# Optimization experiments

Measured on AMD Instinct MI355X. Metric: run time of the kernel, lower is better.

Reference implementation:

```python
import jax, jax.numpy as jnp
import numpy as np

EPS = 1e-5


def conv3x3(x, w, b):
    # x [B,C,H,W], w [O,C,3,3], stride 1, pad 1
    y = jax.lax.conv_general_dilated(x, w, (1, 1), ((1, 1), (1, 1)),
                                     dimension_numbers=('NCHW', 'OIHW', 'NCHW'))
    return y + b[None, :, None, None]


def bilinear_gather(x, py, px):
    # x [B,C,H,W]; sampling locations py,px [B,K,H,W] -> [B,C,K,H,W]
    # Zero padding outside the image (matches deform_conv CUDA semantics:
    # out-of-bound corner values contribute 0).
    B, C, H, W = x.shape
    K = py.shape[1]
    x_flat = x.reshape(B, C, H * W)
    y0 = jnp.floor(py)
    x0 = jnp.floor(px)
    out = jnp.zeros((B, C, K, H, W), x.dtype)
    for dy in (0.0, 1.0):
        for dx in (0.0, 1.0):
            yi = y0 + dy
            xi = x0 + dx
            wgt = (1.0 - jnp.abs(py - yi)) * (1.0 - jnp.abs(px - xi))  # [B,K,H,W]
            valid = (yi >= 0) & (yi <= H - 1) & (xi >= 0) & (xi <= W - 1)
            idx = (jnp.clip(yi, 0, H - 1).astype(jnp.int32) * W
                   + jnp.clip(xi, 0, W - 1).astype(jnp.int32)).reshape(B, -1)
            vals = jax.vmap(lambda xf, i: xf[:, i])(x_flat, idx)  # [B,C,K*H*W]
            out = out + (wgt * valid)[:, None] * vals.reshape(B, C, K, H, W)
    return out


def setup_inputs() -> dict:
    key = jax.random.key(0)
    k1, k2, k3 = jax.random.split(key, 3)
    B, C, O, H, W = 4, 64, 64, 128, 128
    x = jax.random.normal(k1, (B, C, H, W), jnp.float32)
    # offset predictor: small init so predicted offsets are modest (realistic)
    off_w = 0.01 * jax.random.normal(k2, (18, C, 3, 3), jnp.float32)
    off_b = jnp.zeros((18,), jnp.float32)
    dc_w = jax.random.normal(k3, (O, C, 3, 3), jnp.float32) / np.sqrt(C * 9)
    dc_b = jnp.zeros((O,), jnp.float32)
    gamma = jnp.ones((O,), jnp.float32)
    beta = jnp.zeros((O,), jnp.float32)
    return {"x": x, "off_w": off_w, "off_b": off_b, "dc_w": dc_w,
            "dc_b": dc_b, "gamma": gamma, "beta": beta}


def reference(x, off_w, off_b, dc_w, dc_b, gamma, beta):
    B, C, H, W = x.shape
    O = dc_w.shape[0]
    K = 9  # 3x3 kernel
    offset = conv3x3(x, off_w, off_b)              # [B,18,H,W]
    off = offset.reshape(B, K, 2, H, W)            # (dy,dx) per kernel tap, row-major
    dyo, dxo = off[:, :, 0], off[:, :, 1]          # [B,K,H,W]
    k = (jnp.arange(3) - 1).astype(x.dtype)        # kernel taps {-1,0,1}
    kgy = jnp.repeat(k, 3)                         # [9] row-major y offsets
    kgx = jnp.tile(k, 3)                           # [9] row-major x offsets
    hh = jnp.arange(H, dtype=x.dtype)
    ww = jnp.arange(W, dtype=x.dtype)
    # stride 1, pad 1: base point = out_pos - 1 + tap; pad is folded into kgy/kgx
    py = hh[None, None, :, None] + kgy[None, :, None, None] + dyo
    px = ww[None, None, None, :] + kgx[None, :, None, None] + dxo
    sampled = bilinear_gather(x, py, px)           # [B,C,K,H,W]
    y = jnp.einsum('ock,bckhw->bohw', dc_w.reshape(O, C, K), sampled)
    y = y + dc_b[None, :, None, None]
    # BatchNorm2d (training mode: biased batch statistics)
    mu = y.mean(axis=(0, 2, 3), keepdims=True)
    var = y.var(axis=(0, 2, 3), keepdims=True)
    yn = (y - mu) * jax.lax.rsqrt(var + EPS)
    return jax.nn.relu(yn * gamma[None, :, None, None] + beta[None, :, None, None])
```

## Files before the change

kernel.cpp:

```cpp
#include <hip/hip_runtime.h>

#define HH 128
#define WW 128
#define HWSZ (HH * WW)
#define CC 64
#define OO 64
#define BB 4
#define NOFF 18
#define KK 576

#define WS_BG     0
#define WS_BGO    18432
#define WS_SUMS   27648
#define WS_SUMSQ  27712
#define WS_YBUF   27776

typedef __attribute__((ext_vector_type(8))) short short8;
typedef __attribute__((ext_vector_type(4))) int int4v;
typedef __attribute__((ext_vector_type(4))) float f32x4;

__device__ inline unsigned bf16rne(float f) {
  unsigned u = __float_as_uint(f);
  u += 0x7fff + ((u >> 16) & 1);
  return u >> 16;
}

__global__ __launch_bounds__(256) void prep_kernel(
    const float* __restrict__ x, const float* __restrict__ off_w,
    const float* __restrict__ dc_w, unsigned int* __restrict__ xTu,
    int* __restrict__ Bg, int* __restrict__ Bgo, float* __restrict__ sums) {
  int bid = blockIdx.x;
  if (bid < BB * HH) {
    __shared__ float T[CC][WW + 1];
    int b = bid >> 7, h = bid & 127;
    int tw = threadIdx.x & 127, th = threadIdx.x >> 7;
    const float* xp = x + (size_t)b * CC * HWSZ + h * WW;
#pragma unroll 8
    for (int i = 0; i < 32; ++i) {
      int c = i * 2 + th;
      T[c][tw] = xp[c * HWSZ + tw];
    }
    __syncthreads();
    int c2 = threadIdx.x & 31, wq = threadIdx.x >> 5;
    unsigned int* op = xTu + ((size_t)(b * HH + h) * WW) * 32;
#pragma unroll 8
    for (int i = 0; i < 16; ++i) {
      int w = i * 8 + wq;
      unsigned pk = bf16rne(T[2 * c2][w]) | (bf16rne(T[2 * c2 + 1][w]) << 16);
      op[w * 32 + c2] = pk;
    }
  } else {
    int pb = bid - BB * HH;
    int tid = pb * 256 + threadIdx.x;
    int stride = 64 * 256;
    for (int i = tid; i < 72 * 64 * 4; i += stride) {
      int j = i & 3, o = (i >> 2) & 63, g = i >> 8;
      int k2 = g * 4 + j, t = k2 >> 5, jj = k2 & 31;
      unsigned lo = bf16rne(dc_w[o * KK + (2 * jj) * 9 + t]);
      unsigned hi = bf16rne(dc_w[o * KK + (2 * jj + 1) * 9 + t]);
      Bg[i] = (int)(lo | (hi << 16));
    }
    for (int i = tid; i < 72 * 32 * 4; i += stride) {
      int j = i & 3, o = (i >> 2) & 31, g = i >> 7;
      int k2 = g * 4 + j, t = k2 >> 5, jj = k2 & 31;
      unsigned pk = 0;
      if (o < NOFF) {
        unsigned lo = bf16rne(off_w[o * KK + (2 * jj) * 9 + t]);
        unsigned hi = bf16rne(off_w[o * KK + (2 * jj + 1) * 9 + t]);
        pk = lo | (hi << 16);
      }
      Bgo[i] = (int)pk;
    }
    if (tid < 128) sums[tid] = 0.0f;
  }
}

__global__ __launch_bounds__(256) void fused_kernel(
    const unsigned int* __restrict__ xTu, const int* __restrict__ Bg,
    const int* __restrict__ Bgo, const float* __restrict__ off_b,
    const float* __restrict__ dc_b, float* __restrict__ ybuf,
    float* __restrict__ sums, float* __restrict__ sumsq) {
  __shared__ __align__(16) int A[4 * 16 * 100];
  __shared__ __align__(16) int M[4 * 144 * 4];
  __shared__ float offL[4][NOFF][16];

  int cg = threadIdx.x >> 6, lane = threadIdx.x & 63;
  int b = blockIdx.x >> 8, rem = blockIdx.x & 255;
  int h = rem >> 1, w0 = (rem & 1) * 64;
  int hw0 = h * WW + w0;
  int p0 = cg * 16;
  int n16 = lane & 15, q = lane >> 4;
  int pg = lane >> 3, part = lane & 7;
  const unsigned int* xbu = xTu + (size_t)b * HWSZ * 32;

  f32x4 acc2[2] = {f32x4{0, 0, 0, 0}, f32x4{0, 0, 0, 0}};
#pragma unroll 1
  for (int chunk = 0; chunk < 3; ++chunk) {
    int cy = h + chunk - 1;
    bool vy = (cy >= 0) && (cy < HH);
    int cys = min(max(cy, 0), HH - 1);
#pragma unroll
    for (int tl = 0; tl < 3; ++tl) {
#pragma unroll
      for (int i = 0; i < 2; ++i) {
        int px = i * 8 + pg;
        int cx = w0 + p0 + px + tl - 1;
        bool v = vy && (cx >= 0) && (cx < WW);
        int cxs = min(max(cx, 0), WW - 1);
        int4v val = *(const int4v*)&xbu[(cys * WW + cxs) * 32 + part * 4];
        if (!v) { val.x = 0; val.y = 0; val.z = 0; val.w = 0; }
        *(int4v*)&A[(p0 + px) * 100 + tl * 32 + part * 4] = val;
      }
    }
#pragma unroll 1
    for (int kk = 0; kk < 6; ++kk) {
      int4v av = *(const int4v*)&A[(p0 + n16) * 100 + kk * 16 + q * 4];
      short8 af = __builtin_bit_cast(short8, av);
      int g = chunk * 24 + kk * 4 + q;
#pragma unroll
      for (int nt = 0; nt < 2; ++nt) {
        int4v bv = *(const int4v*)&Bgo[(g * 32 + nt * 16 + n16) * 4];
        short8 bfr = __builtin_bit_cast(short8, bv);
        acc2[nt] = __builtin_amdgcn_mfma_f32_16x16x32_bf16(af, bfr, acc2[nt], 0, 0, 0);
      }
    }
  }
#pragma unroll
  for (int nt = 0; nt < 2; ++nt) {
    int o = nt * 16 + n16;
    if (o < NOFF) {
      float bv = off_b[o];
#pragma unroll
      for (int r = 0; r < 4; ++r) offL[cg][o][q * 4 + r] = acc2[nt][r] + bv;
    }
  }

  int* Mw = M + cg * 144 * 4;
#pragma unroll
  for (int it = 0; it < 3; ++it) {
    int m = it * 64 + lane;
    if (m < 144) {
      int pxl = (unsigned)m / 9u;
      int t = m - pxl * 9;
      float dy = offL[cg][2 * t][pxl];
      float dx = offL[cg][2 * t + 1][pxl];
      float py = (float)(h + t / 3 - 1) + dy;
      float pxf = (float)(w0 + p0 + pxl + (t % 3) - 1) + dx;
      float fy0 = floorf(py), fx0 = floorf(pxf);
      float ay = py - fy0, ax = pxf - fx0;
      int iy0 = (int)fy0, ix0 = (int)fx0;
      int iy1 = iy0 + 1, ix1 = ix0 + 1;
      float wy0 = 1.0f - ay, wy1 = ay, wx0 = 1.0f - ax, wx1 = ax;
      if (!(iy0 >= 0 && iy0 < HH)) wy0 = 0.0f;
      if (!(iy1 >= 0 && iy1 < HH)) wy1 = 0.0f;
      if (!(ix0 >= 0 && ix0 < WW)) wx0 = 0.0f;
      if (!(ix1 >= 0 && ix1 < WW)) wx1 = 0.0f;
      int cy0 = min(max(iy0, 0), HH - 1), cy1 = min(max(iy1, 0), HH - 1);
      int cx0 = min(max(ix0, 0), WW - 1), cx1 = min(max(ix1, 0), WW - 1);
      int4v mv;
      mv.x = (cy0 * WW + cx0) | ((cy0 * WW + cx1) << 16);
      mv.y = (cy1 * WW + cx0) | ((cy1 * WW + cx1) << 16);
      mv.z = (int)(bf16rne(wy0 * wx0) | (bf16rne(wy0 * wx1) << 16));
      mv.w = (int)(bf16rne(wy1 * wx0) | (bf16rne(wy1 * wx1) << 16));
      *(int4v*)&Mw[m * 4] = mv;
    }
  }

  int p = lane >> 5;
  int c2 = lane & 31;
  f32x4 acc[4] = {f32x4{0,0,0,0}, f32x4{0,0,0,0}, f32x4{0,0,0,0}, f32x4{0,0,0,0}};
#pragma unroll 1
  for (int chunk = 0; chunk < 3; ++chunk) {
#pragma unroll 1
    for (int tl = 0; tl < 3; ++tl) {
#pragma unroll 4
      for (int pp = 0; pp < 16; pp += 2) {
        int pxl = pp + p;
        int4v mv = *(const int4v*)&Mw[(pxl * 9 + chunk * 3 + tl) * 4];
        unsigned o00 = mv.x & 0xffff, o01 = ((unsigned)mv.x) >> 16;
        unsigned o10 = mv.y & 0xffff, o11 = ((unsigned)mv.y) >> 16;
        unsigned d00 = xbu[o00 * 32 + c2];
        unsigned d01 = xbu[o01 * 32 + c2];
        unsigned d10 = xbu[o10 * 32 + c2];
        unsigned d11 = xbu[o11 * 32 + c2];
        float w00 = __uint_as_float(((unsigned)mv.z) << 16);
        float w01 = __uint_as_float(((unsigned)mv.z) & 0xffff0000u);
        float w10 = __uint_as_float(((unsigned)mv.w) << 16);
        float w11 = __uint_as_float(((unsigned)mv.w) & 0xffff0000u);
        float slo = w00 * __uint_as_float(d00 << 16);
        slo = fmaf(w01, __uint_as_float(d01 << 16), slo);
        slo = fmaf(w10, __uint_as_float(d10 << 16), slo);
        slo = fmaf(w11, __uint_as_float(d11 << 16), slo);
        float shi = w00 * __uint_as_float(d00 & 0xffff0000u);
        shi = fmaf(w01, __uint_as_float(d01 & 0xffff0000u), shi);
        shi = fmaf(w10, __uint_as_float(d10 & 0xffff0000u), shi);
        shi = fmaf(w11, __uint_as_float(d11 & 0xffff0000u), shi);
        unsigned pk = __builtin_amdgcn_perm(
            __float_as_uint(shi) + 0x8000u,
            __float_as_uint(slo) + 0x8000u, 0x07060302u);
        A[(p0 + pxl) * 100 + tl * 32 + c2] = (int)pk;
      }
    }
#pragma unroll 1
    for (int kk = 0; kk < 6; ++kk) {
      int4v av = *(const int4v*)&A[(p0 + n16) * 100 + kk * 16 + q * 4];
      short8 af = __builtin_bit_cast(short8, av);
      int g = chunk * 24 + kk * 4 + q;
#pragma unroll
      for (int nt = 0; nt < 4; ++nt) {
        int4v bv = *(const int4v*)&Bg[(g * 64 + nt * 16 + n16) * 4];
        short8 bfr = __builtin_bit_cast(short8, bv);
        acc[nt] = __builtin_amdgcn_mfma_f32_16x16x32_bf16(af, bfr, acc[nt], 0, 0, 0);
      }
    }
  }

  float* SW = (float*)&A[cg * 1600];
#pragma unroll
  for (int nt = 0; nt < 4; ++nt) {
    int o = nt * 16 + n16;
    float bv = dc_b[o];
    f32x4 r;
    float s = 0.0f, ss = 0.0f;
#pragma unroll
    for (int r0 = 0; r0 < 4; ++r0) {
      r[r0] = acc[nt][r0] + bv;
      s += r[r0];
      ss += r[r0] * r[r0];
    }
    *(f32x4*)(ybuf + (size_t)(b * OO + o) * HWSZ + hw0 + p0 + q * 4) = r;
    s += __shfl_xor(s, 16);  s += __shfl_xor(s, 32);
    ss += __shfl_xor(ss, 16); ss += __shfl_xor(ss, 32);
    if (lane < 16) {
      SW[nt * 16 + lane] = s;
      SW[64 + nt * 16 + lane] = ss;
    }
  }
  __syncthreads();
  if (threadIdx.x < 64) {
    float ts = 0.0f, tq = 0.0f;
#pragma unroll
    for (int wv = 0; wv < 4; ++wv) {
      const float* Sv = (const float*)&A[wv * 1600];
      ts += Sv[threadIdx.x];
      tq += Sv[64 + threadIdx.x];
    }
    atomicAdd(&sums[threadIdx.x], ts);
    atomicAdd(&sumsq[threadIdx.x], tq);
  }
}

__global__ __launch_bounds__(256) void norm_kernel(
    const float* __restrict__ ybuf, const float* __restrict__ sums,
    const float* __restrict__ sumsq, const float* __restrict__ gamma,
    const float* __restrict__ beta, float* __restrict__ out) {
  int gid = blockIdx.x * 256 + threadIdx.x;
  int flat = gid << 2;
  int o = (flat >> 14) & 63;
  const float invN = 1.0f / (float)(BB * HWSZ);
  float mean = sums[o] * invN;
  float var = sumsq[o] * invN - mean * mean;
  float rstd = rsqrtf(var + 1e-5f);
  float g = gamma[o] * rstd;
  float bta = beta[o] - mean * g;
  float4 v = ((const float4*)ybuf)[gid];
  float4 r;
  r.x = fmaxf(v.x * g + bta, 0.0f);
  r.y = fmaxf(v.y * g + bta, 0.0f);
  r.z = fmaxf(v.z * g + bta, 0.0f);
  r.w = fmaxf(v.w * g + bta, 0.0f);
  ((float4*)out)[gid] = r;
}

extern "C" void kernel_launch(void* const* d_in, const int* in_sizes, int n_in,
                              void* d_out, int out_size, void* d_ws, size_t ws_size,
                              hipStream_t stream) {
  const float* x     = (const float*)d_in[0];
  const float* off_w = (const float*)d_in[1];
  const float* off_b = (const float*)d_in[2];
  const float* dc_w  = (const float*)d_in[3];
  const float* dc_b  = (const float*)d_in[4];
  const float* gamma = (const float*)d_in[5];
  const float* beta  = (const float*)d_in[6];
  float* ws = (float*)d_ws;
  int*   Bg     = (int*)(ws + WS_BG);
  int*   Bgo    = (int*)(ws + WS_BGO);
  float* sums   = ws + WS_SUMS;
  float* sumsq  = ws + WS_SUMSQ;
  float* ybuf   = ws + WS_YBUF;
  float* out = (float*)d_out;
  unsigned int* xTu = (unsigned int*)d_out;

  prep_kernel<<<BB * HH + 64, 256, 0, stream>>>(x, off_w, dc_w, xTu, Bg, Bgo, sums);
  fused_kernel<<<BB * HWSZ / 64, 256, 0, stream>>>(xTu, Bg, Bgo, off_b, dc_b, ybuf, sums, sumsq);
  norm_kernel<<<BB * OO * HWSZ / (4 * 256), 256, 0, stream>>>(ybuf, sums, sumsq, gamma, beta, out);
}
```

Before: 141.8 us.

## Fuse prep, conv and batchnorm into one cooperative kernel with grid syncs

Merges the three launches into one cooperative kernel that separates the prep, deformable-conv and normalisation stages with grid-wide syncs. Conv accumulators stay in registers across the second sync, so the intermediate pre-norm output buffer is never written to or read back from global memory. Each wave also starts its chunk loop at a different row offset, to spread concurrent loads across rows. The cost is that all 1024 blocks must be co-resident, which depends on the LDS union and occupancy fitting; otherwise it falls back to the multi-kernel path.

```diff
diff --git a/kernel.cpp b/kernel.cpp
--- a/kernel.cpp
+++ b/kernel.cpp
@@ -1,4 +1,5 @@
 #include <hip/hip_runtime.h>
+#include <hip/hip_cooperative_groups.h>
 
 #define HH 128
 #define WW 128
@@ -8,6 +9,7 @@
 #define BB 4
 #define NOFF 18
 #define KK 576
+#define EPS 1e-5f
 
 #define WS_BG     0
 #define WS_BGO    18432
@@ -19,48 +21,58 @@
 typedef __attribute__((ext_vector_type(4))) int int4v;
 typedef __attribute__((ext_vector_type(4))) float f32x4;
 
+struct SM {
+  union {
+    struct {
+      int A[4 * 16 * 100];
+      int M[4 * 144 * 4];
+      float offL[4][NOFF][16];
+    } c;
+    float T[CC][WW + 1];
+  };
+};
+
 __device__ inline unsigned bf16rne(float f) {
   unsigned u = __float_as_uint(f);
   u += 0x7fff + ((u >> 16) & 1);
   return u >> 16;
 }
 
-__global__ __launch_bounds__(256) void prep_kernel(
-    const float* __restrict__ x, const float* __restrict__ off_w,
-    const float* __restrict__ dc_w, unsigned int* __restrict__ xTu,
-    int* __restrict__ Bg, int* __restrict__ Bgo, float* __restrict__ sums) {
-  int bid = blockIdx.x;
+__device__ void stage_prep(const float* __restrict__ x,
+                           const float* __restrict__ off_w,
+                           const float* __restrict__ dc_w,
+                           unsigned int* __restrict__ xTu,
+                           int* __restrict__ Bg, int* __restrict__ Bgo,
+                           float* __restrict__ sums, SM& sm, int bid, int tid) {
   if (bid < BB * HH) {
-    __shared__ float T[CC][WW + 1];
     int b = bid >> 7, h = bid & 127;
-    int tw = threadIdx.x & 127, th = threadIdx.x >> 7;
+    int tw = tid & 127, th = tid >> 7;
     const float* xp = x + (size_t)b * CC * HWSZ + h * WW;
 #pragma unroll 8
     for (int i = 0; i < 32; ++i) {
       int c = i * 2 + th;
-      T[c][tw] = xp[c * HWSZ + tw];
+      sm.T[c][tw] = xp[c * HWSZ + tw];
     }
     __syncthreads();
-    int c2 = threadIdx.x & 31, wq = threadIdx.x >> 5;
+    int c2 = tid & 31, wq = tid >> 5;
     unsigned int* op = xTu + ((size_t)(b * HH + h) * WW) * 32;
 #pragma unroll 8
     for (int i = 0; i < 16; ++i) {
       int w = i * 8 + wq;
-      unsigned pk = bf16rne(T[2 * c2][w]) | (bf16rne(T[2 * c2 + 1][w]) << 16);
+      unsigned pk = bf16rne(sm.T[2 * c2][w]) | (bf16rne(sm.T[2 * c2 + 1][w]) << 16);
       op[w * 32 + c2] = pk;
     }
-  } else {
-    int pb = bid - BB * HH;
-    int tid = pb * 256 + threadIdx.x;
-    int stride = 64 * 256;
-    for (int i = tid; i < 72 * 64 * 4; i += stride) {
+  } else if (bid < BB * HH + 64) {
+    int t0 = (bid - BB * HH) * 256 + tid;
+    const int stride = 64 * 256;
+    for (int i = t0; i < 72 * 64 * 4; i += stride) {
       int j = i & 3, o = (i >> 2) & 63, g = i >> 8;
       int k2 = g * 4 + j, t = k2 >> 5, jj = k2 & 31;
       unsigned lo = bf16rne(dc_w[o * KK + (2 * jj) * 9 + t]);
       unsigned hi = bf16rne(dc_w[o * KK + (2 * jj + 1) * 9 + t]);
       Bg[i] = (int)(lo | (hi << 16));
     }
-    for (int i = tid; i < 72 * 32 * 4; i += stride) {
+    for (int i = t0; i < 72 * 32 * 4; i += stride) {
       int j = i & 3, o = (i >> 2) & 31, g = i >> 7;
       int k2 = g * 4 + j, t = k2 >> 5, jj = k2 & 31;
       unsigned pk = 0;
@@ -71,21 +83,20 @@
       }
       Bgo[i] = (int)pk;
     }
-    if (tid < 128) sums[tid] = 0.0f;
-  }
-}
-
-__global__ __launch_bounds__(256) void fused_kernel(
-    const unsigned int* __restrict__ xTu, const int* __restrict__ Bg,
-    const int* __restrict__ Bgo, const float* __restrict__ off_b,
-    const float* __restrict__ dc_b, float* __restrict__ ybuf,
-    float* __restrict__ sums, float* __restrict__ sumsq) {
-  __shared__ __align__(16) int A[4 * 16 * 100];
-  __shared__ __align__(16) int M[4 * 144 * 4];
-  __shared__ float offL[4][NOFF][16];
-
-  int cg = threadIdx.x >> 6, lane = threadIdx.x & 63;
-  int b = blockIdx.x >> 8, rem = blockIdx.x & 255;
+    if (t0 < 128)
+      __hip_atomic_store(&sums[t0], 0.0f, __ATOMIC_RELAXED, __HIP_MEMORY_SCOPE_AGENT);
+  }
+}
+
+__device__ void stage_conv(const unsigned int* __restrict__ xTu,
+                           const int* __restrict__ Bg, const int* __restrict__ Bgo,
+                           const float* __restrict__ off_b,
+                           const float* __restrict__ dc_b,
+                           float* __restrict__ sums, float* __restrict__ sumsq,
+                           float* __restrict__ ybuf, SM& sm, int bid, int tid,
+                           f32x4 (&acc)[4]) {
+  int cg = tid >> 6, lane = tid & 63;
+  int b = bid >> 8, rem = bid & 255;
   int h = rem >> 1, w0 = (rem & 1) * 64;
   int hw0 = h * WW + w0;
   int p0 = cg * 16;
@@ -95,7 +106,10 @@
 
   f32x4 acc2[2] = {f32x4{0, 0, 0, 0}, f32x4{0, 0, 0, 0}};
 #pragma unroll 1
-  for (int chunk = 0; chunk < 3; ++chunk) {
+  for (int cc = 0; cc < 3; ++cc) {
+    int chunk = cc + cg;
+    chunk = (chunk >= 3) ? chunk - 3 : chunk;
+    chunk = (chunk >= 3) ? chunk - 3 : chunk;
     int cy = h + chunk - 1;
     bool vy = (cy >= 0) && (cy < HH);
     int cys = min(max(cy, 0), HH - 1);
@@ -109,12 +123,12 @@
         int cxs = min(max(cx, 0), WW - 1);
         int4v val = *(const int4v*)&xbu[(cys * WW + cxs) * 32 + part * 4];
         if (!v) { val.x = 0; val.y = 0; val.z = 0; val.w = 0; }
-        *(int4v*)&A[(p0 + px) * 100 + tl * 32 + part * 4] = val;
+        *(int4v*)&sm.c.A[(p0 + px) * 100 + tl * 32 + part * 4] = val;
       }
     }
 #pragma unroll 1
     for (int kk = 0; kk < 6; ++kk) {
-      int4v av = *(const int4v*)&A[(p0 + n16) * 100 + kk * 16 + q * 4];
+      int4v av = *(const int4v*)&sm.c.A[(p0 + n16) * 100 + kk * 16 + q * 4];
       short8 af = __builtin_bit_cast(short8, av);
       int g = chunk * 24 + kk * 4 + q;
 #pragma unroll
@@ -131,19 +145,19 @@
     if (o < NOFF) {
       float bv = off_b[o];
 #pragma unroll
-      for (int r = 0; r < 4; ++r) offL[cg][o][q * 4 + r] = acc2[nt][r] + bv;
-    }
-  }
-
-  int* Mw = M + cg * 144 * 4;
+      for (int r = 0; r < 4; ++r) sm.c.offL[cg][o][q * 4 + r] = acc2[nt][r] + bv;
+    }
+  }
+
+  int* Mw = sm.c.M + cg * 144 * 4;
 #pragma unroll
   for (int it = 0; it < 3; ++it) {
     int m = it * 64 + lane;
     if (m < 144) {
       int pxl = (unsigned)m / 9u;
       int t = m - pxl * 9;
-      float dy = offL[cg][2 * t][pxl];
-      float dx = offL[cg][2 * t + 1][pxl];
+      float dy = sm.c.offL[cg][2 * t][pxl];
+      float dx = sm.c.offL[cg][2 * t + 1][pxl];
       float py = (float)(h + t / 3 - 1) + dy;
       float pxf = (float)(w0 + p0 + pxl + (t % 3) - 1) + dx;
       float fy0 = floorf(py), fx0 = floorf(pxf);
@@ -168,9 +182,13 @@
 
   int p = lane >> 5;
   int c2 = lane & 31;
-  f32x4 acc[4] = {f32x4{0,0,0,0}, f32x4{0,0,0,0}, f32x4{0,0,0,0}, f32x4{0,0,0,0}};
-#pragma unroll 1
-  for (int chunk = 0; chunk < 3; ++chunk) {
+#pragma unroll
+  for (int nt = 0; nt < 4; ++nt) acc[nt] = f32x4{0, 0, 0, 0};
+#pragma unroll 1
+  for (int cc = 0; cc < 3; ++cc) {
+    int chunk = cc + cg;
+    chunk = (chunk >= 3) ? chunk - 3 : chunk;
+    chunk = (chunk >= 3) ? chunk - 3 : chunk;
 #pragma unroll 1
     for (int tl = 0; tl < 3; ++tl) {
 #pragma unroll 4
@@ -198,12 +216,12 @@
         unsigned pk = __builtin_amdgcn_perm(
             __float_as_uint(shi) + 0x8000u,
             __float_as_uint(slo) + 0x8000u, 0x07060302u);
-        A[(p0 + pxl) * 100 + tl * 32 + c2] = (int)pk;
+        sm.c.A[(p0 + pxl) * 100 + tl * 32 + c2] = (int)pk;
       }
     }
 #pragma unroll 1
     for (int kk = 0; kk < 6; ++kk) {
-      int4v av = *(const int4v*)&A[(p0 + n16) * 100 + kk * 16 + q * 4];
+      int4v av = *(const int4v*)&sm.c.A[(p0 + n16) * 100 + kk * 16 + q * 4];
       short8 af = __builtin_bit_cast(short8, av);
       int g = chunk * 24 + kk * 4 + q;
 #pragma unroll
@@ -215,20 +233,20 @@
     }
   }
 
-  float* SW = (float*)&A[cg * 1600];
+  float* SW = (float*)&sm.c.A[cg * 1600];
 #pragma unroll
   for (int nt = 0; nt < 4; ++nt) {
     int o = nt * 16 + n16;
     float bv = dc_b[o];
-    f32x4 r;
     float s = 0.0f, ss = 0.0f;
 #pragma unroll
     for (int r0 = 0; r0 < 4; ++r0) {
-      r[r0] = acc[nt][r0] + bv;
-      s += r[r0];
-      ss += r[r0] * r[r0];
-    }
-    *(f32x4*)(ybuf + (size_t)(b * OO + o) * HWSZ + hw0 + p0 + q * 4) = r;
+      acc[nt][r0] += bv;
+      s += acc[nt][r0];
+      ss += acc[nt][r0] * acc[nt][r0];
+    }
+    if (ybuf)
+      *(f32x4*)(ybuf + (size_t)(b * OO + o) * HWSZ + hw0 + p0 + q * 4) = acc[nt];
     s += __shfl_xor(s, 16);  s += __shfl_xor(s, 32);
     ss += __shfl_xor(ss, 16); ss += __shfl_xor(ss, 32);
     if (lane < 16) {
@@ -237,17 +255,83 @@
     }
   }
   __syncthreads();
-  if (threadIdx.x < 64) {
+  if (tid < 64) {
     float ts = 0.0f, tq = 0.0f;
 #pragma unroll
     for (int wv = 0; wv < 4; ++wv) {
-      const float* Sv = (const float*)&A[wv * 1600];
-      ts += Sv[threadIdx.x];
-      tq += Sv[64 + threadIdx.x];
-    }
-    atomicAdd(&sums[threadIdx.x], ts);
-    atomicAdd(&sumsq[threadIdx.x], tq);
-  }
+      const float* Sv = (const float*)&sm.c.A[wv * 1600];
+      ts += Sv[tid];
+      tq += Sv[64 + tid];
+    }
+    atomicAdd(&sums[tid], ts);
+    atomicAdd(&sumsq[tid], tq);
+  }
+}
+
+__device__ void stage_norm(int bid, int tid, const f32x4 (&acc)[4],
+                           const float* __restrict__ sums,
+                           const float* __restrict__ sumsq,
+                           const float* __restrict__ gamma,
+                           const float* __restrict__ beta,
+                           float* __restrict__ out) {
+  int cg = tid >> 6, lane = tid & 63;
+  int b = bid >> 8, rem = bid & 255;
+  int h = rem >> 1, w0 = (rem & 1) * 64;
+  int hw0 = h * WW + w0;
+  int p0 = cg * 16;
+  int n16 = lane & 15, q = lane >> 4;
+  const float invN = 1.0f / (float)(BB * HWSZ);
+#pragma unroll
+  for (int nt = 0; nt < 4; ++nt) {
+    int o = nt * 16 + n16;
+    float sv = __hip_atomic_load(&sums[o], __ATOMIC_RELAXED, __HIP_MEMORY_SCOPE_AGENT);
+    float qv = __hip_atomic_load(&sumsq[o], __ATOMIC_RELAXED, __HIP_MEMORY_SCOPE_AGENT);
+    float mean = sv * invN;
+    float var = qv * invN - mean * mean;
+    float rstd = rsqrtf(var + EPS);
+    float g = gamma[o] * rstd;
+    float bta = beta[o] - mean * g;
+    f32x4 r;
+#pragma unroll
+    for (int r0 = 0; r0 < 4; ++r0) r[r0] = fmaxf(acc[nt][r0] * g + bta, 0.0f);
+    *(f32x4*)(out + (size_t)(b * OO + o) * HWSZ + hw0 + p0 + q * 4) = r;
+  }
+}
+
+__global__ __launch_bounds__(256) void coop_kernel(
+    const float* __restrict__ x, const float* __restrict__ off_w,
+    const float* __restrict__ dc_w, const float* __restrict__ off_b,
+    const float* __restrict__ dc_b, const float* __restrict__ gamma,
+    const float* __restrict__ beta, unsigned int* __restrict__ xTu,
+    int* __restrict__ Bg, int* __restrict__ Bgo, float* __restrict__ sums,
+    float* __restrict__ sumsq, float* __restrict__ out) {
+  __shared__ SM sm;
+  int bid = blockIdx.x, tid = threadIdx.x;
+  stage_prep(x, off_w, dc_w, xTu, Bg, Bgo, sums, sm, bid, tid);
+  cooperative_groups::this_grid().sync();
+  f32x4 acc[4];
+  stage_conv(xTu, Bg, Bgo, off_b, dc_b, sums, sumsq, nullptr, sm, bid, tid, acc);
+  cooperative_groups::this_grid().sync();
+  stage_norm(bid, tid, acc, sums, sumsq, gamma, beta, out);
+}
+
+__global__ __launch_bounds__(256) void prep_kernel(
+    const float* __restrict__ x, const float* __restrict__ off_w,
+    const float* __restrict__ dc_w, unsigned int* __restrict__ xTu,
+    int* __restrict__ Bg, int* __restrict__ Bgo, float* __restrict__ sums) {
+  __shared__ SM sm;
+  stage_prep(x, off_w, dc_w, xTu, Bg, Bgo, sums, sm, blockIdx.x, threadIdx.x);
+}
+
+__global__ __launch_bounds__(256) void conv_kernel(
+    const unsigned int* __restrict__ xTu, const int* __restrict__ Bg,
+    const int* __restrict__ Bgo, const float* __restrict__ off_b,
+    const float* __restrict__ dc_b, float* __restrict__ ybuf,
+    float* __restrict__ sums, float* __restrict__ sumsq) {
+  __shared__ SM sm;
+  f32x4 acc[4];
+  stage_conv(xTu, Bg, Bgo, off_b, dc_b, sums, sumsq, ybuf, sm, blockIdx.x,
+             threadIdx.x, acc);
 }
 
 __global__ __launch_bounds__(256) void norm_kernel(
@@ -260,7 +344,7 @@
   const float invN = 1.0f / (float)(BB * HWSZ);
   float mean = sums[o] * invN;
   float var = sumsq[o] * invN - mean * mean;
-  float rstd = rsqrtf(var + 1e-5f);
+  float rstd = rsqrtf(var + EPS);
   float g = gamma[o] * rstd;
   float bta = beta[o] - mean * g;
   float4 v = ((const float4*)ybuf)[gid];
@@ -283,15 +367,30 @@
   const float* gamma = (const float*)d_in[5];
   const float* beta  = (const float*)d_in[6];
   float* ws = (float*)d_ws;
-  int*   Bg     = (int*)(ws + WS_BG);
-  int*   Bgo    = (int*)(ws + WS_BGO);
-  float* sums   = ws + WS_SUMS;
-  float* sumsq  = ws + WS_SUMSQ;
-  float* ybuf   = ws + WS_YBUF;
+  int*   Bg    = (int*)(ws + WS_BG);
+  int*   Bgo   = (int*)(ws + WS_BGO);
+  float* sums  = ws + WS_SUMS;
+  float* sumsq = ws + WS_SUMSQ;
+  float* ybuf  = ws + WS_YBUF;
   float* out = (float*)d_out;
   unsigned int* xTu = (unsigned int*)d_out;
 
+  int nb = 0;
+  hipError_t qe = hipOccupancyMaxActiveBlocksPerMultiprocessor(
+      &nb, reinterpret_cast<const void*>(coop_kernel), 256, 0);
+  bool coop_ok = (qe == hipSuccess) && (nb >= 4);
+
+  if (coop_ok) {
+    void* args[] = {(void*)&x, (void*)&off_w, (void*)&dc_w, (void*)&off_b,
+                    (void*)&dc_b, (void*)&gamma, (void*)&beta, (void*)&xTu,
+                    (void*)&Bg, (void*)&Bgo, (void*)&sums, (void*)&sumsq,
+                    (void*)&out};
+    hipError_t le = hipLaunchCooperativeKernel(
+        reinterpret_cast<const void*>(coop_kernel), dim3(BB * HWSZ / 64),
+        dim3(256), args, 0, stream);
+    if (le == hipSuccess) return;
+  }
   prep_kernel<<<BB * HH + 64, 256, 0, stream>>>(x, off_w, dc_w, xTu, Bg, Bgo, sums);
-  fused_kernel<<<BB * HWSZ / 64, 256, 0, stream>>>(xTu, Bg, Bgo, off_b, dc_b, ybuf, sums, sumsq);
+  conv_kernel<<<BB * HWSZ / 64, 256, 0, stream>>>(xTu, Bg, Bgo, off_b, dc_b, ybuf, sums, sumsq);
   norm_kernel<<<BB * OO * HWSZ / (4 * 256), 256, 0, stream>>>(ybuf, sums, sumsq, gamma, beta, out);
 }
```

Measured after the change: 155.6 us. 9.7% more time.

## Build MFMA A-fragments directly in registers, dropping shared-memory staging

Applied to the files above, without the earlier changes.

The offset conv and the deformable sampling stage now load each lane's bf16 channel slice straight from global memory into the MFMA A operand, instead of staging through a shared A tile. The bilinear interpolation is vectorized: each lane fetches 16-byte channel groups for its pixel and uses packed 2-wide float math. This removes the shared-memory writes and reads and their bank traffic, and shrinks LDS use. In exchange, each lane does more gather loads and holds more registers, and wide loads from scattered sample positions may coalesce worse.

```diff
diff --git a/kernel.cpp b/kernel.cpp
--- a/kernel.cpp
+++ b/kernel.cpp
@@ -8,6 +8,7 @@
 #define BB 4
 #define NOFF 18
 #define KK 576
+#define EPS 1e-5f
 
 #define WS_BG     0
 #define WS_BGO    18432
@@ -18,20 +19,31 @@
 typedef __attribute__((ext_vector_type(8))) short short8;
 typedef __attribute__((ext_vector_type(4))) int int4v;
 typedef __attribute__((ext_vector_type(4))) float f32x4;
+typedef __attribute__((ext_vector_type(2))) float f32x2;
 
 __device__ inline unsigned bf16rne(float f) {
   unsigned u = __float_as_uint(f);
   u += 0x7fff + ((u >> 16) & 1);
   return u >> 16;
 }
+__device__ inline f32x2 up2(unsigned d) {
+  f32x2 r;
+  r.x = __uint_as_float(d << 16);
+  r.y = __uint_as_float(d & 0xffff0000u);
+  return r;
+}
+__device__ inline unsigned pk2(f32x2 s) {
+  return __builtin_amdgcn_perm(__float_as_uint(s.y) + 0x8000u,
+                               __float_as_uint(s.x) + 0x8000u, 0x07060302u);
+}
 
 __global__ __launch_bounds__(256) void prep_kernel(
     const float* __restrict__ x, const float* __restrict__ off_w,
     const float* __restrict__ dc_w, unsigned int* __restrict__ xTu,
     int* __restrict__ Bg, int* __restrict__ Bgo, float* __restrict__ sums) {
+  __shared__ float T[CC][WW + 1];
   int bid = blockIdx.x;
   if (bid < BB * HH) {
-    __shared__ float T[CC][WW + 1];
     int b = bid >> 7, h = bid & 127;
     int tw = threadIdx.x & 127, th = threadIdx.x >> 7;
     const float* xp = x + (size_t)b * CC * HWSZ + h * WW;
@@ -50,17 +62,16 @@
       op[w * 32 + c2] = pk;
     }
   } else {
-    int pb = bid - BB * HH;
-    int tid = pb * 256 + threadIdx.x;
-    int stride = 64 * 256;
-    for (int i = tid; i < 72 * 64 * 4; i += stride) {
+    int t0 = (bid - BB * HH) * 256 + threadIdx.x;
+    const int stride = 64 * 256;
+    for (int i = t0; i < 72 * 64 * 4; i += stride) {
       int j = i & 3, o = (i >> 2) & 63, g = i >> 8;
       int k2 = g * 4 + j, t = k2 >> 5, jj = k2 & 31;
       unsigned lo = bf16rne(dc_w[o * KK + (2 * jj) * 9 + t]);
       unsigned hi = bf16rne(dc_w[o * KK + (2 * jj + 1) * 9 + t]);
       Bg[i] = (int)(lo | (hi << 16));
     }
-    for (int i = tid; i < 72 * 32 * 4; i += stride) {
+    for (int i = t0; i < 72 * 32 * 4; i += stride) {
       int j = i & 3, o = (i >> 2) & 31, g = i >> 7;
       int k2 = g * 4 + j, t = k2 >> 5, jj = k2 & 31;
       unsigned pk = 0;
@@ -71,18 +82,18 @@
       }
       Bgo[i] = (int)pk;
     }
-    if (tid < 128) sums[tid] = 0.0f;
-  }
-}
-
-__global__ __launch_bounds__(256) void fused_kernel(
+    if (t0 < 128) sums[t0] = 0.0f;
+  }
+}
+
+__global__ __launch_bounds__(256) void conv_kernel(
     const unsigned int* __restrict__ xTu, const int* __restrict__ Bg,
     const int* __restrict__ Bgo, const float* __restrict__ off_b,
     const float* __restrict__ dc_b, float* __restrict__ ybuf,
     float* __restrict__ sums, float* __restrict__ sumsq) {
-  __shared__ __align__(16) int A[4 * 16 * 100];
   __shared__ __align__(16) int M[4 * 144 * 4];
   __shared__ float offL[4][NOFF][16];
+  __shared__ float Ssum[256], Ssq[256];
 
   int cg = threadIdx.x >> 6, lane = threadIdx.x & 63;
   int b = blockIdx.x >> 8, rem = blockIdx.x & 255;
@@ -90,10 +101,10 @@
   int hw0 = h * WW + w0;
   int p0 = cg * 16;
   int n16 = lane & 15, q = lane >> 4;
-  int pg = lane >> 3, part = lane & 7;
   const unsigned int* xbu = xTu + (size_t)b * HWSZ * 32;
 
   f32x4 acc2[2] = {f32x4{0, 0, 0, 0}, f32x4{0, 0, 0, 0}};
+  int cxp = w0 + p0 + n16 - 1;
 #pragma unroll 1
   for (int chunk = 0; chunk < 3; ++chunk) {
     int cy = h + chunk - 1;
@@ -101,27 +112,23 @@
     int cys = min(max(cy, 0), HH - 1);
 #pragma unroll
     for (int tl = 0; tl < 3; ++tl) {
-#pragma unroll
-      for (int i = 0; i < 2; ++i) {
-        int px = i * 8 + pg;
-        int cx = w0 + p0 + px + tl - 1;
-        bool v = vy && (cx >= 0) && (cx < WW);
-        int cxs = min(max(cx, 0), WW - 1);
-        int4v val = *(const int4v*)&xbu[(cys * WW + cxs) * 32 + part * 4];
-        if (!v) { val.x = 0; val.y = 0; val.z = 0; val.w = 0; }
-        *(int4v*)&A[(p0 + px) * 100 + tl * 32 + part * 4] = val;
-      }
-    }
-#pragma unroll 1
-    for (int kk = 0; kk < 6; ++kk) {
-      int4v av = *(const int4v*)&A[(p0 + n16) * 100 + kk * 16 + q * 4];
-      short8 af = __builtin_bit_cast(short8, av);
-      int g = chunk * 24 + kk * 4 + q;
-#pragma unroll
-      for (int nt = 0; nt < 2; ++nt) {
-        int4v bv = *(const int4v*)&Bgo[(g * 32 + nt * 16 + n16) * 4];
-        short8 bfr = __builtin_bit_cast(short8, bv);
-        acc2[nt] = __builtin_amdgcn_mfma_f32_16x16x32_bf16(af, bfr, acc2[nt], 0, 0, 0);
+      int cx = cxp + tl;
+      bool v = vy && (cx >= 0) && (cx < WW);
+      int cxs = min(max(cx, 0), WW - 1);
+      const unsigned int* src = xbu + (cys * WW + cxs) * 32 + q * 4;
+      int t = chunk * 3 + tl;
+#pragma unroll
+      for (int s = 0; s < 2; ++s) {
+        int4v av = *(const int4v*)(src + s * 16);
+        if (!v) { av.x = 0; av.y = 0; av.z = 0; av.w = 0; }
+        short8 af = __builtin_bit_cast(short8, av);
+        int g = (t * 2 + s) * 4 + q;
+#pragma unroll
+        for (int nt = 0; nt < 2; ++nt) {
+          int4v bv = *(const int4v*)&Bgo[(g * 32 + nt * 16 + n16) * 4];
+          short8 bfr = __builtin_bit_cast(short8, bv);
+          acc2[nt] = __builtin_amdgcn_mfma_f32_16x16x32_bf16(af, bfr, acc2[nt], 0, 0, 0);
+        }
       }
     }
   }
@@ -166,46 +173,57 @@
     }
   }
 
-  int p = lane >> 5;
-  int c2 = lane & 31;
   f32x4 acc[4] = {f32x4{0,0,0,0}, f32x4{0,0,0,0}, f32x4{0,0,0,0}, f32x4{0,0,0,0}};
 #pragma unroll 1
-  for (int chunk = 0; chunk < 3; ++chunk) {
-#pragma unroll 1
-    for (int tl = 0; tl < 3; ++tl) {
-#pragma unroll 4
-      for (int pp = 0; pp < 16; pp += 2) {
-        int pxl = pp + p;
-        int4v mv = *(const int4v*)&Mw[(pxl * 9 + chunk * 3 + tl) * 4];
-        unsigned o00 = mv.x & 0xffff, o01 = ((unsigned)mv.x) >> 16;
-        unsigned o10 = mv.y & 0xffff, o11 = ((unsigned)mv.y) >> 16;
-        unsigned d00 = xbu[o00 * 32 + c2];
-        unsigned d01 = xbu[o01 * 32 + c2];
-        unsigned d10 = xbu[o10 * 32 + c2];
-        unsigned d11 = xbu[o11 * 32 + c2];
-        float w00 = __uint_as_float(((unsigned)mv.z) << 16);
-        float w01 = __uint_as_float(((unsigned)mv.z) & 0xffff0000u);
-        float w10 = __uint_as_float(((unsigned)mv.w) << 16);
-        float w11 = __uint_as_float(((unsigned)mv.w) & 0xffff0000u);
-        float slo = w00 * __uint_as_float(d00 << 16);
-        slo = fmaf(w01, __uint_as_float(d01 << 16), slo);
-        slo = fmaf(w10, __uint_as_float(d10 << 16), slo);
-        slo = fmaf(w11, __uint_as_float(d11 << 16), slo);
-        float shi = w00 * __uint_as_float(d00 & 0xffff0000u);
-        shi = fmaf(w01, __uint_as_float(d01 & 0xffff0000u), shi);
-        shi = fmaf(w10, __uint_as_float(d10 & 0xffff0000u), shi);
-        shi = fmaf(w11, __uint_as_float(d11 & 0xffff0000u), shi);
-        unsigned pk = __builtin_amdgcn_perm(
-            __float_as_uint(shi) + 0x8000u,
-            __float_as_uint(slo) + 0x8000u, 0x07060302u);
-        A[(p0 + pxl) * 100 + tl * 32 + c2] = (int)pk;
-      }
-    }
-#pragma unroll 1
-    for (int kk = 0; kk < 6; ++kk) {
-      int4v av = *(const int4v*)&A[(p0 + n16) * 100 + kk * 16 + q * 4];
+  for (int t = 0; t < 9; ++t) {
+    int4v mv = *(const int4v*)&Mw[(n16 * 9 + t) * 4];
+    unsigned o00 = mv.x & 0xffff, o01 = ((unsigned)mv.x) >> 16;
+    unsigned o10 = mv.y & 0xffff, o11 = ((unsigned)mv.y) >> 16;
+    f32x2 w00; w00.x = __uint_as_float(((unsigned)mv.z) << 16);        w00.y = w00.x;
+    f32x2 w01; w01.x = __uint_as_float(((unsigned)mv.z) & 0xffff0000u); w01.y = w01.x;
+    f32x2 w10; w10.x = __uint_as_float(((unsigned)mv.w) << 16);        w10.y = w10.x;
+    f32x2 w11; w11.x = __uint_as_float(((unsigned)mv.w) & 0xffff0000u); w11.y = w11.x;
+    const unsigned int* p00 = xbu + o00 * 32 + q * 4;
+    const unsigned int* p01 = xbu + o01 * 32 + q * 4;
+    const unsigned int* p10 = xbu + o10 * 32 + q * 4;
+    const unsigned int* p11 = xbu + o11 * 32 + q * 4;
+#pragma unroll
+    for (int s = 0; s < 2; ++s) {
+      int4v d00 = *(const int4v*)(p00 + s * 16);
+      int4v d01 = *(const int4v*)(p01 + s * 16);
+      int4v d10 = *(const int4v*)(p10 + s * 16);
+      int4v d11 = *(const int4v*)(p11 + s * 16);
+      int4v av;
+      {
+        f32x2 sc = up2(d00.x) * w00;
+        sc = up2(d01.x) * w01 + sc;
+        sc = up2(d10.x) * w10 + sc;
+        sc = up2(d11.x) * w11 + sc;
+        av.x = (int)pk2(sc);
+      }
+      {
+        f32x2 sc = up2(d00.y) * w00;
+        sc = up2(d01.y) * w01 + sc;
+        sc = up2(d10.y) * w10 + sc;
+        sc = up2(d11.y) * w11 + sc;
+        av.y = (int)pk2(sc);
+      }
+      {
+        f32x2 sc = up2(d00.z) * w00;
+        sc = up2(d01.z) * w01 + sc;
+        sc = up2(d10.z) * w10 + sc;
+        sc = up2(d11.z) * w11 + sc;
+        av.z = (int)pk2(sc);
+      }
+      {
+        f32x2 sc = up2(d00.w) * w00;
+        sc = up2(d01.w) * w01 + sc;
+        sc = up2(d10.w) * w10 + sc;
+        sc = up2(d11.w) * w11 + sc;
+        av.w = (int)pk2(sc);
+      }
       short8 af = __builtin_bit_cast(short8, av);
-      int g = chunk * 24 + kk * 4 + q;
+      int g = (t * 2 + s) * 4 + q;
 #pragma unroll
       for (int nt = 0; nt < 4; ++nt) {
         int4v bv = *(const int4v*)&Bg[(g * 64 + nt * 16 + n16) * 4];
@@ -215,25 +233,23 @@
     }
   }
 
-  float* SW = (float*)&A[cg * 1600];
 #pragma unroll
   for (int nt = 0; nt < 4; ++nt) {
     int o = nt * 16 + n16;
     float bv = dc_b[o];
-    f32x4 r;
     float s = 0.0f, ss = 0.0f;
 #pragma unroll
     for (int r0 = 0; r0 < 4; ++r0) {
-      r[r0] = acc[nt][r0] + bv;
-      s += r[r0];
-      ss += r[r0] * r[r0];
-    }
-    *(f32x4*)(ybuf + (size_t)(b * OO + o) * HWSZ + hw0 + p0 + q * 4) = r;
+      acc[nt][r0] += bv;
+      s += acc[nt][r0];
+      ss += acc[nt][r0] * acc[nt][r0];
+    }
+    *(f32x4*)(ybuf + (size_t)(b * OO + o) * HWSZ + hw0 + p0 + q * 4) = acc[nt];
     s += __shfl_xor(s, 16);  s += __shfl_xor(s, 32);
     ss += __shfl_xor(ss, 16); ss += __shfl_xor(ss, 32);
     if (lane < 16) {
-      SW[nt * 16 + lane] = s;
-      SW[64 + nt * 16 + lane] = ss;
+      Ssum[cg * 64 + nt * 16 + lane] = s;
+      Ssq[cg * 64 + nt * 16 + lane] = ss;
     }
   }
   __syncthreads();
@@ -241,9 +257,8 @@
     float ts = 0.0f, tq = 0.0f;
 #pragma unroll
     for (int wv = 0; wv < 4; ++wv) {
-      const float* Sv = (const float*)&A[wv * 1600];
-      ts += Sv[threadIdx.x];
-      tq += Sv[64 + threadIdx.x];
+      ts += Ssum[wv * 64 + threadIdx.x];
+      tq += Ssq[wv * 64 + threadIdx.x];
     }
     atomicAdd(&sums[threadIdx.x], ts);
     atomicAdd(&sumsq[threadIdx.x], tq);
@@ -260,7 +275,7 @@
   const float invN = 1.0f / (float)(BB * HWSZ);
   float mean = sums[o] * invN;
   float var = sumsq[o] * invN - mean * mean;
-  float rstd = rsqrtf(var + 1e-5f);
+  float rstd = rsqrtf(var + EPS);
   float g = gamma[o] * rstd;
   float bta = beta[o] - mean * g;
   float4 v = ((const float4*)ybuf)[gid];
@@ -283,15 +298,15 @@
   const float* gamma = (const float*)d_in[5];
   const float* beta  = (const float*)d_in[6];
   float* ws = (float*)d_ws;
-  int*   Bg     = (int*)(ws + WS_BG);
-  int*   Bgo    = (int*)(ws + WS_BGO);
-  float* sums   = ws + WS_SUMS;
-  float* sumsq  = ws + WS_SUMSQ;
-  float* ybuf   = ws + WS_YBUF;
+  int*   Bg    = (int*)(ws + WS_BG);
+  int*   Bgo   = (int*)(ws + WS_BGO);
+  float* sums  = ws + WS_SUMS;
+  float* sumsq = ws + WS_SUMSQ;
+  float* ybuf  = ws + WS_YBUF;
   float* out = (float*)d_out;
   unsigned int* xTu = (unsigned int*)d_out;
 
   prep_kernel<<<BB * HH + 64, 256, 0, stream>>>(x, off_w, dc_w, xTu, Bg, Bgo, sums);
-  fused_kernel<<<BB * HWSZ / 64, 256, 0, stream>>>(xTu, Bg, Bgo, off_b, dc_b, ybuf, sums, sumsq);
+  conv_kernel<<<BB * HWSZ / 64, 256, 0, stream>>>(xTu, Bg, Bgo, off_b, dc_b, ybuf, sums, sumsq);
   norm_kernel<<<BB * OO * HWSZ / (4 * 256), 256, 0, stream>>>(ybuf, sums, sumsq, gamma, beta, out);
 }
```

New measurement: 166.5 us. 1.17x slower.
